# Optimization experiments

Measured on AMD Instinct MI355X. Metric: run time of the kernel, lower is better.

The kernel has to match this reference:

```python
import jax, jax.numpy as jnp
import numpy as np

TOP_K = 2
N_TOKENS = 8192
D_IN = 2048
HIDDEN = 2048
N_EXPERTS = 8


def setup_inputs() -> dict:
    key = jax.random.key(0)
    ks = jax.random.split(key, 3)
    # 0.001 stddev matches RandomNormal(mean=0, stddev=0.001) initializers
    x = jax.random.normal(ks[0], (N_TOKENS, D_IN), dtype=jnp.float32)
    Wg = jax.random.normal(ks[1], (D_IN, N_EXPERTS), dtype=jnp.float32) * 0.001
    bg = jnp.zeros((N_EXPERTS,), dtype=jnp.float32)
    We = jax.random.normal(ks[2], (N_EXPERTS, D_IN, HIDDEN), dtype=jnp.float32) * 0.001
    be = jnp.zeros((N_EXPERTS, HIDDEN), dtype=jnp.float32)
    return {"x": x, "Wg": Wg, "bg": bg, "We": We, "be": be}


def reference(x, Wg, bg, We, be):
    # Gating: dense -> softmax over experts
    gating = jax.nn.softmax(x @ Wg + bg, axis=-1)          # [N, E]
    top_w, top_i = jax.lax.top_k(gating, TOP_K)            # [N, K] each
    # Dense all-expert compute (as in the original: every expert runs on every token)
    expert_out = jnp.einsum('nd,edh->neh', x, We) + be      # [N, E, H]
    # Gather the top-k expert outputs per token and combine with gating weights
    sel = jnp.take_along_axis(expert_out, top_i[:, :, None], axis=1)  # [N, K, H]
    combined = jnp.sum(sel * top_w[:, :, None], axis=1)    # [N, H]
    return combined
```

## Files before the change

kernel.cpp:

```cpp
#include <hip/hip_runtime.h>
#include <hip/hip_bf16.h>

#define N_TOKENS 8192
#define D_IN     2048
#define HIDDEN   2048
#define N_EXP    8
#define CAP      N_TOKENS
#define GATE_BLOCKS 256
#define TPOSE_BLOCKS (N_EXP * 32 * 32)

typedef __bf16 bf16x8 __attribute__((ext_vector_type(8)));
typedef float  f32x4  __attribute__((ext_vector_type(4)));

#define OFF_CNT   0
#define OFF_TOK   4096
#define OFF_W     266240
#define OFF_XBF   1048576
#define OFF_WET   34603008

__device__ __forceinline__ unsigned short f2bf(float f) {
  unsigned int u = __builtin_bit_cast(unsigned int, f);
  u += 0x7fffu + ((u >> 16) & 1u);
  return (unsigned short)(u >> 16);
}

__device__ __forceinline__ void g2l16(const void* g, void* l) {
  __builtin_amdgcn_global_load_lds(
      (__attribute__((address_space(1))) void*)g,
      (__attribute__((address_space(3))) void*)l, 16, 0, 0);
}

union PrepSM {
  float tile[64][68];
  struct {
    int   lcnt[8];
    int   base[8];
    int   ltok[8][32];
    float lw[8][32];
  } g;
};

__global__ __launch_bounds__(256) void prep_kernel(
    const float* __restrict__ x, const float* __restrict__ Wg,
    const float* __restrict__ bg, const float* __restrict__ We,
    unsigned short* __restrict__ xbf, unsigned short* __restrict__ wet,
    int* __restrict__ cnt, int* __restrict__ btok, float* __restrict__ bw)
{
  __shared__ PrepSM sm;
  const int tid = threadIdx.x;

  if (blockIdx.x >= GATE_BLOCKS) {
    const int id = blockIdx.x - GATE_BLOCKS;
    const int e  = id >> 10;
    const int rem = id & 1023;
    const int d0 = (rem >> 5) << 6;
    const int h0 = (rem & 31) << 6;
    const int r  = tid >> 2;
    const int g  = tid & 3;

    const float* src = We + ((size_t)e * D_IN + d0 + r) * HIDDEN + h0 + g * 16;
#pragma unroll
    for (int i = 0; i < 4; ++i)
      *(float4*)&sm.tile[r][g * 16 + i * 4] = *(const float4*)(src + i * 4);
    __syncthreads();

    union { unsigned short s[16]; uint4 q[2]; } u;
#pragma unroll
    for (int i = 0; i < 16; ++i) u.s[i] = f2bf(sm.tile[g * 16 + i][r]);
    uint4* dst = (uint4*)(wet + ((size_t)e * HIDDEN + h0 + r) * D_IN + d0 + g * 16);
    dst[0] = u.q[0];
    dst[1] = u.q[1];
    return;
  }

  const int lane = tid & 63;
  const int wid  = tid >> 6;
  if (tid < 8) sm.g.lcnt[tid] = 0;
  __syncthreads();

  const int tb = blockIdx.x * 32 + wid * 8;
  for (int tk = 0; tk < 8; ++tk) {
    const int n = tb + tk;
    const float* xr = x + (size_t)n * D_IN;
    unsigned short* xbr = xbf + (size_t)n * D_IN;

#pragma unroll
    for (int c = 0; c < 8; ++c) {
      const int d = c * 256 + lane * 4;
      float4 xv = *(const float4*)(xr + d);
      uint2 pk;
      pk.x = (unsigned int)f2bf(xv.x) | ((unsigned int)f2bf(xv.y) << 16);
      pk.y = (unsigned int)f2bf(xv.z) | ((unsigned int)f2bf(xv.w) << 16);
      *(uint2*)(xbr + d) = pk;
    }

    float acc[8];
#pragma unroll
    for (int e = 0; e < 8; ++e) acc[e] = 0.f;
#pragma unroll 4
    for (int c = 0; c < 32; ++c) {
      const int d = c * 64 + lane;
      const float xv = xr[d];
      const float4 g0 = *(const float4*)(Wg + (size_t)d * 8);
      const float4 g1 = *(const float4*)(Wg + (size_t)d * 8 + 4);
      acc[0] += xv * g0.x; acc[1] += xv * g0.y;
      acc[2] += xv * g0.z; acc[3] += xv * g0.w;
      acc[4] += xv * g1.x; acc[5] += xv * g1.y;
      acc[6] += xv * g1.z; acc[7] += xv * g1.w;
    }
#pragma unroll
    for (int e = 0; e < 8; ++e) {
      float v = acc[e];
      v += __shfl_down(v, 32); v += __shfl_down(v, 16); v += __shfl_down(v, 8);
      v += __shfl_down(v, 4);  v += __shfl_down(v, 2);  v += __shfl_down(v, 1);
      acc[e] = v;
    }

    if (lane == 0) {
      float lg[8], p[8];
      float mx = -1e30f;
#pragma unroll
      for (int e = 0; e < 8; ++e) { lg[e] = acc[e] + bg[e]; mx = fmaxf(mx, lg[e]); }
      float s = 0.f;
#pragma unroll
      for (int e = 0; e < 8; ++e) { p[e] = expf(lg[e] - mx); s += p[e]; }
      const float inv = 1.f / s;
      int e1 = 0;
#pragma unroll
      for (int e = 1; e < 8; ++e) if (lg[e] > lg[e1]) e1 = e;
      int e2 = (e1 == 0) ? 1 : 0;
#pragma unroll
      for (int e = 0; e < 8; ++e) if (e != e1 && lg[e] > lg[e2]) e2 = e;

      const int s1 = atomicAdd(&sm.g.lcnt[e1], 1);
      sm.g.ltok[e1][s1] = n;  sm.g.lw[e1][s1] = p[e1] * inv;
      const int s2 = atomicAdd(&sm.g.lcnt[e2], 1);
      sm.g.ltok[e2][s2] = n;  sm.g.lw[e2][s2] = p[e2] * inv;
    }
  }
  __syncthreads();

  if (tid < 8) sm.g.base[tid] = atomicAdd(&cnt[tid * 32], sm.g.lcnt[tid]);
  __syncthreads();

  const int e = tid >> 5, i = tid & 31;
  if (i < sm.g.lcnt[e]) {
    const int o = e * CAP + sm.g.base[e] + i;
    btok[o] = sm.g.ltok[e][i];
    bw[o]   = sm.g.lw[e][i];
  }
}

__global__ __launch_bounds__(256, 4) void moe_gemm(
    const unsigned short* __restrict__ xbf, const unsigned short* __restrict__ wet,
    const float* __restrict__ be, const int* __restrict__ cnt,
    const int* __restrict__ btok, const float* __restrict__ bw,
    float* __restrict__ out)
{
  const int e  = blockIdx.z;
  const int M  = cnt[e * 32];
  const int m0 = blockIdx.y * 128;
  if (m0 >= M) return;
  const int h0 = blockIdx.x * 128;

  __shared__ __align__(16) unsigned short As[128 * 64];
  __shared__ __align__(16) unsigned short Bs[128 * 64];

  const int tid  = threadIdx.x;
  const int wid  = tid >> 6;
  const int lane = tid & 63;
  const int wm   = wid >> 1;
  const int wn   = wid & 1;

  const int* etok = btok + e * CAP;
  const float* ew = bw + e * CAP;

  const int kcs = (((lane & 7) ^ (lane >> 3)) * 8);

  size_t asrc[4], bsrc[4];
#pragma unroll
  for (int j = 0; j < 4; ++j) {
    const int c = wid * 4 + j;
    const int r = c * 8 + (lane >> 3);
    int ar = m0 + r;
    if (ar >= M) ar = m0;
    const int tok = etok[ar];
    asrc[j] = (size_t)tok * D_IN + kcs;
    bsrc[j] = ((size_t)e * HIDDEN + h0 + r) * D_IN + kcs;
  }

  f32x4 acc[4][4];
#pragma unroll
  for (int i = 0; i < 4; ++i)
#pragma unroll
    for (int j = 0; j < 4; ++j) acc[i][j] = (f32x4){0.f, 0.f, 0.f, 0.f};

  for (int k0 = 0; k0 < D_IN; k0 += 64) {
    __syncthreads();
#pragma unroll
    for (int j = 0; j < 4; ++j)
      g2l16(xbf + asrc[j] + k0, &As[(wid * 4 + j) * 512]);
#pragma unroll
    for (int j = 0; j < 4; ++j)
      g2l16(wet + bsrc[j] + k0, &Bs[(wid * 4 + j) * 512]);
    __syncthreads();

#pragma unroll
    for (int kh = 0; kh < 2; ++kh) {
      bf16x8 af[4], bfr[4];
#pragma unroll
      for (int fm = 0; fm < 4; ++fm) {
        const int row = wm * 64 + fm * 16 + (lane & 15);
        const int kc  = kh * 4 + (lane >> 4);
        af[fm] = __builtin_bit_cast(bf16x8,
            *(const uint4*)(As + row * 64 + ((kc ^ (row & 7)) * 8)));
      }
#pragma unroll
      for (int fn = 0; fn < 4; ++fn) {
        const int row = wn * 64 + fn * 16 + (lane & 15);
        const int kc  = kh * 4 + (lane >> 4);
        bfr[fn] = __builtin_bit_cast(bf16x8,
            *(const uint4*)(Bs + row * 64 + ((kc ^ (row & 7)) * 8)));
      }
#pragma unroll
      for (int fm = 0; fm < 4; ++fm)
#pragma unroll
        for (int fn = 0; fn < 4; ++fn)
          acc[fm][fn] = __builtin_amdgcn_mfma_f32_16x16x32_bf16(
              af[fm], bfr[fn], acc[fm][fn], 0, 0, 0);
    }
  }

  float bias[4];
#pragma unroll
  for (int fn = 0; fn < 4; ++fn)
    bias[fn] = be[e * HIDDEN + h0 + wn * 64 + fn * 16 + (lane & 15)];

#pragma unroll
  for (int fm = 0; fm < 4; ++fm) {
    const int rbase = m0 + wm * 64 + fm * 16 + (lane >> 4) * 4;
#pragma unroll
    for (int reg = 0; reg < 4; ++reg) {
      const int r = rbase + reg;
      if (r < M) {
        const int tok = etok[r];
        const float w = ew[r];
        float* orow = out + (size_t)tok * HIDDEN + h0 + wn * 64 + (lane & 15);
#pragma unroll
        for (int fn = 0; fn < 4; ++fn)
          atomicAdd(orow + fn * 16, w * (acc[fm][fn][reg] + bias[fn]));
      }
    }
  }
}

extern "C" void kernel_launch(void* const* d_in, const int* in_sizes, int n_in,
                              void* d_out, int out_size, void* d_ws, size_t ws_size,
                              hipStream_t stream) {
  const float* x  = (const float*)d_in[0];
  const float* Wg = (const float*)d_in[1];
  const float* bg = (const float*)d_in[2];
  const float* We = (const float*)d_in[3];
  const float* be = (const float*)d_in[4];
  float* out = (float*)d_out;

  char* ws = (char*)d_ws;
  int*            cnt  = (int*)(ws + OFF_CNT);
  int*            btok = (int*)(ws + OFF_TOK);
  float*          bw   = (float*)(ws + OFF_W);
  unsigned short* xbf  = (unsigned short*)(ws + OFF_XBF);
  unsigned short* wet  = (unsigned short*)(ws + OFF_WET);

  hipMemsetAsync(d_out, 0, (size_t)out_size * sizeof(float), stream);
  hipMemsetAsync(cnt, 0, 8 * 32 * sizeof(int), stream);

  prep_kernel<<<GATE_BLOCKS + TPOSE_BLOCKS, 256, 0, stream>>>(
      x, Wg, bg, We, xbf, wet, cnt, btok, bw);
  moe_gemm<<<dim3(HIDDEN / 128, N_TOKENS / 128, N_EXP), 256, 0, stream>>>(
      xbf, wet, be, cnt, btok, bw, out);
}
```

Before: 530.9 us.

## Double-buffer LDS tiles in MoE GEMM with prefetch two steps ahead

Converts the GEMM main loop to a double-buffered LDS pipeline. Direct global-to-LDS loads for tile t+2 are issued right after the fragments of tile t are read into registers, so the MFMAs run while the next tiles are in flight. It uses explicit vmcnt/lgkmcnt waits, raw barriers, sched_barriers and setprio around the MFMA block. LDS use doubles and launch bounds drop from 4 to 2 blocks per CU, which can reduce occupancy. The last two iterations issue wasted loads that wrap back to k=0.

```diff
diff --git a/kernel.cpp b/kernel.cpp
--- a/kernel.cpp
+++ b/kernel.cpp
@@ -151,7 +151,7 @@
   }
 }
 
-__global__ __launch_bounds__(256, 4) void moe_gemm(
+__global__ __launch_bounds__(256, 2) void moe_gemm(
     const unsigned short* __restrict__ xbf, const unsigned short* __restrict__ wet,
     const float* __restrict__ be, const int* __restrict__ cnt,
     const int* __restrict__ btok, const float* __restrict__ bw,
@@ -163,8 +163,8 @@
   if (m0 >= M) return;
   const int h0 = blockIdx.x * 128;
 
-  __shared__ __align__(16) unsigned short As[128 * 64];
-  __shared__ __align__(16) unsigned short Bs[128 * 64];
+  __shared__ __align__(16) unsigned short As[2][128 * 64];
+  __shared__ __align__(16) unsigned short Bs[2][128 * 64];
 
   const int tid  = threadIdx.x;
   const int wid  = tid >> 6;
@@ -195,40 +195,74 @@
 #pragma unroll
     for (int j = 0; j < 4; ++j) acc[i][j] = (f32x4){0.f, 0.f, 0.f, 0.f};
 
-  for (int k0 = 0; k0 < D_IN; k0 += 64) {
-    __syncthreads();
-#pragma unroll
-    for (int j = 0; j < 4; ++j)
-      g2l16(xbf + asrc[j] + k0, &As[(wid * 4 + j) * 512]);
-#pragma unroll
-    for (int j = 0; j < 4; ++j)
-      g2l16(wet + bsrc[j] + k0, &Bs[(wid * 4 + j) * 512]);
-    __syncthreads();
-
+#pragma unroll
+  for (int j = 0; j < 4; ++j)
+    g2l16(xbf + asrc[j], &As[0][(wid * 4 + j) * 512]);
+#pragma unroll
+  for (int j = 0; j < 4; ++j)
+    g2l16(wet + bsrc[j], &Bs[0][(wid * 4 + j) * 512]);
+  asm volatile("" ::: "memory");
+#pragma unroll
+  for (int j = 0; j < 4; ++j)
+    g2l16(xbf + asrc[j] + 64, &As[1][(wid * 4 + j) * 512]);
+#pragma unroll
+  for (int j = 0; j < 4; ++j)
+    g2l16(wet + bsrc[j] + 64, &Bs[1][(wid * 4 + j) * 512]);
+
+#pragma unroll 1
+  for (int t = 0; t < D_IN / 64; ++t) {
+    const int cur = t & 1;
+    const unsigned short* Ab = &As[cur][0];
+    const unsigned short* Bb = &Bs[cur][0];
+
+    asm volatile("s_waitcnt vmcnt(8)" ::: "memory");
+    __builtin_amdgcn_s_barrier();
+    __builtin_amdgcn_sched_barrier(0);
+
+    bf16x8 af[4][2], bfr[4][2];
 #pragma unroll
     for (int kh = 0; kh < 2; ++kh) {
-      bf16x8 af[4], bfr[4];
 #pragma unroll
       for (int fm = 0; fm < 4; ++fm) {
         const int row = wm * 64 + fm * 16 + (lane & 15);
         const int kc  = kh * 4 + (lane >> 4);
-        af[fm] = __builtin_bit_cast(bf16x8,
-            *(const uint4*)(As + row * 64 + ((kc ^ (row & 7)) * 8)));
+        af[fm][kh] = __builtin_bit_cast(bf16x8,
+            *(const uint4*)(Ab + row * 64 + ((kc ^ (row & 7)) * 8)));
       }
 #pragma unroll
       for (int fn = 0; fn < 4; ++fn) {
         const int row = wn * 64 + fn * 16 + (lane & 15);
         const int kc  = kh * 4 + (lane >> 4);
-        bfr[fn] = __builtin_bit_cast(bf16x8,
-            *(const uint4*)(Bs + row * 64 + ((kc ^ (row & 7)) * 8)));
+        bfr[fn][kh] = __builtin_bit_cast(bf16x8,
+            *(const uint4*)(Bb + row * 64 + ((kc ^ (row & 7)) * 8)));
       }
+    }
+
+    asm volatile("s_waitcnt lgkmcnt(0)" ::: "memory");
+    __builtin_amdgcn_sched_barrier(0);
+    __builtin_amdgcn_s_barrier();
+    __builtin_amdgcn_sched_barrier(0);
+
+    int kp = (t + 2) * 64;
+    if (kp >= D_IN) kp = 0;
+#pragma unroll
+    for (int j = 0; j < 4; ++j)
+      g2l16(xbf + asrc[j] + kp, &As[cur][(wid * 4 + j) * 512]);
+#pragma unroll
+    for (int j = 0; j < 4; ++j)
+      g2l16(wet + bsrc[j] + kp, &Bs[cur][(wid * 4 + j) * 512]);
+    __builtin_amdgcn_sched_barrier(0);
+
+    __builtin_amdgcn_s_setprio(1);
+#pragma unroll
+    for (int kh = 0; kh < 2; ++kh)
 #pragma unroll
       for (int fm = 0; fm < 4; ++fm)
 #pragma unroll
         for (int fn = 0; fn < 4; ++fn)
           acc[fm][fn] = __builtin_amdgcn_mfma_f32_16x16x32_bf16(
-              af[fm], bfr[fn], acc[fm][fn], 0, 0, 0);
-    }
+              af[fm][kh], bfr[fn][kh], acc[fm][fn], 0, 0, 0);
+    __builtin_amdgcn_s_setprio(0);
   }
 
   float bias[4];
```

Measured after the change: 576.6 us. +8.6%, slower.

## Enlarge MoE GEMM tiles to 256x256 with multi-stage LDS prefetch pipeline

Applied to the files above, without the earlier changes.

Rewrites the grouped expert GEMM to use 512-thread blocks computing 256x256 output tiles with 8 waves. The K loop now runs over 32-wide k-slices held in a four-slot LDS ring (double buffer by two slices), issuing async global-to-LDS loads several slices ahead and interleaving them with MFMA bursts under explicit waitcnt and barrier control. The aim is to hide global load latency and raise arithmetic intensity per LDS byte. Costs include higher register pressure from 32 accumulator tiles, coarser tiles that waste work on partial expert groups, and a fragile hand-scheduled pipeline.

```diff
diff --git a/kernel.cpp b/kernel.cpp
--- a/kernel.cpp
+++ b/kernel.cpp
@@ -151,7 +151,7 @@
   }
 }
 
-__global__ __launch_bounds__(256, 4) void moe_gemm(
+__global__ __launch_bounds__(512, 2) void moe_gemm(
     const unsigned short* __restrict__ xbf, const unsigned short* __restrict__ wet,
     const float* __restrict__ be, const int* __restrict__ cnt,
     const int* __restrict__ btok, const float* __restrict__ bw,
@@ -159,76 +159,107 @@
 {
   const int e  = blockIdx.z;
   const int M  = cnt[e * 32];
-  const int m0 = blockIdx.y * 128;
+  const int m0 = blockIdx.y * 256;
   if (m0 >= M) return;
-  const int h0 = blockIdx.x * 128;
-
-  __shared__ __align__(16) unsigned short As[128 * 64];
-  __shared__ __align__(16) unsigned short Bs[128 * 64];
+  const int h0 = blockIdx.x * 256;
+
+  __shared__ __align__(16) unsigned short As[2][2][256 * 32];
+  __shared__ __align__(16) unsigned short Bs[2][2][256 * 32];
 
   const int tid  = threadIdx.x;
   const int wid  = tid >> 6;
   const int lane = tid & 63;
-  const int wm   = wid >> 1;
-  const int wn   = wid & 1;
+  const int wm   = wid >> 2;
+  const int wn   = wid & 3;
 
   const int* etok = btok + e * CAP;
   const float* ew = bw + e * CAP;
 
-  const int kcs = (((lane & 7) ^ (lane >> 3)) * 8);
-
-  size_t asrc[4], bsrc[4];
-#pragma unroll
-  for (int j = 0; j < 4; ++j) {
-    const int c = wid * 4 + j;
-    const int r = c * 8 + (lane >> 3);
+  const int kqs = (((lane & 3) ^ ((lane >> 3) & 3)) * 8);
+
+  size_t asrc[2], bsrc[2];
+#pragma unroll
+  for (int j = 0; j < 2; ++j) {
+    const int r = (wid * 2 + j) * 16 + (lane >> 2);
     int ar = m0 + r;
     if (ar >= M) ar = m0;
-    const int tok = etok[ar];
-    asrc[j] = (size_t)tok * D_IN + kcs;
-    bsrc[j] = ((size_t)e * HIDDEN + h0 + r) * D_IN + kcs;
-  }
-
-  f32x4 acc[4][4];
-#pragma unroll
-  for (int i = 0; i < 4; ++i)
+    asrc[j] = (size_t)etok[ar] * D_IN + kqs;
+    bsrc[j] = ((size_t)e * HIDDEN + h0 + r) * D_IN + kqs;
+  }
+
+  f32x4 acc[8][4];
+#pragma unroll
+  for (int i = 0; i < 8; ++i)
 #pragma unroll
     for (int j = 0; j < 4; ++j) acc[i][j] = (f32x4){0.f, 0.f, 0.f, 0.f};
 
-  for (int k0 = 0; k0 < D_IN; k0 += 64) {
-    __syncthreads();
-#pragma unroll
-    for (int j = 0; j < 4; ++j)
-      g2l16(xbf + asrc[j] + k0, &As[(wid * 4 + j) * 512]);
-#pragma unroll
-    for (int j = 0; j < 4; ++j)
-      g2l16(wet + bsrc[j] + k0, &Bs[(wid * 4 + j) * 512]);
-    __syncthreads();
-
-#pragma unroll
-    for (int kh = 0; kh < 2; ++kh) {
-      bf16x8 af[4], bfr[4];
-#pragma unroll
-      for (int fm = 0; fm < 4; ++fm) {
-        const int row = wm * 64 + fm * 16 + (lane & 15);
-        const int kc  = kh * 4 + (lane >> 4);
-        af[fm] = __builtin_bit_cast(bf16x8,
-            *(const uint4*)(As + row * 64 + ((kc ^ (row & 7)) * 8)));
-      }
-#pragma unroll
-      for (int fn = 0; fn < 4; ++fn) {
-        const int row = wn * 64 + fn * 16 + (lane & 15);
-        const int kc  = kh * 4 + (lane >> 4);
-        bfr[fn] = __builtin_bit_cast(bf16x8,
-            *(const uint4*)(Bs + row * 64 + ((kc ^ (row & 7)) * 8)));
-      }
-#pragma unroll
-      for (int fm = 0; fm < 4; ++fm)
-#pragma unroll
-        for (int fn = 0; fn < 4; ++fn)
-          acc[fm][fn] = __builtin_amdgcn_mfma_f32_16x16x32_bf16(
-              af[fm], bfr[fn], acc[fm][fn], 0, 0, 0);
-    }
+  bf16x8 af[8], bfr[4];
+
+#define SG_A(db_, ks_, ko_) {                                                  \
+    const int ko = ((ko_) < D_IN) ? (ko_) : 0;                                 \
+    g2l16(xbf + asrc[0] + ko, &As[db_][ks_][(wid * 2 + 0) * 512]);             \
+    g2l16(xbf + asrc[1] + ko, &As[db_][ks_][(wid * 2 + 1) * 512]);             \
+    asm volatile("" ::: "memory"); }
+#define SG_B(db_, ks_, ko_) {                                                  \
+    const int ko = ((ko_) < D_IN) ? (ko_) : 0;                                 \
+    g2l16(wet + bsrc[0] + ko, &Bs[db_][ks_][(wid * 2 + 0) * 512]);             \
+    g2l16(wet + bsrc[1] + ko, &Bs[db_][ks_][(wid * 2 + 1) * 512]);             \
+    asm volatile("" ::: "memory"); }
+#define RD_A(db_, ks_) {                                                       \
+    _Pragma("unroll")                                                          \
+    for (int fm = 0; fm < 8; ++fm) {                                           \
+      const int row = wm * 128 + fm * 16 + (lane & 15);                        \
+      af[fm] = __builtin_bit_cast(bf16x8, *(const uint4*)(                     \
+          &As[db_][ks_][row * 32 + (((lane >> 4) ^ ((row >> 1) & 3)) * 8)]));} }
+#define RD_B(db_, ks_, nh_) {                                                  \
+    _Pragma("unroll")                                                          \
+    for (int q = 0; q < 2; ++q) {                                              \
+      const int fn = (nh_) * 2 + q;                                            \
+      const int row = wn * 64 + fn * 16 + (lane & 15);                         \
+      bfr[fn] = __builtin_bit_cast(bf16x8, *(const uint4*)(                    \
+          &Bs[db_][ks_][row * 32 + (((lane >> 4) ^ ((row >> 1) & 3)) * 8)]));} }
+#define VM8()  asm volatile("s_waitcnt vmcnt(8)" ::: "memory")
+#define SBAR() { __builtin_amdgcn_sched_barrier(0);                            \
+                 __builtin_amdgcn_s_barrier();                                 \
+                 __builtin_amdgcn_sched_barrier(0); }
+#define LGKM0() { asm volatile("s_waitcnt lgkmcnt(0)" ::: "memory");           \
+                  __builtin_amdgcn_sched_barrier(0); }
+#define MM(nh_) {                                                              \
+    __builtin_amdgcn_s_setprio(1);                                             \
+    _Pragma("unroll")                                                          \
+    for (int fm = 0; fm < 8; ++fm) {                                           \
+      acc[fm][(nh_) * 2] = __builtin_amdgcn_mfma_f32_16x16x32_bf16(            \
+          af[fm], bfr[(nh_) * 2], acc[fm][(nh_) * 2], 0, 0, 0);                \
+      acc[fm][(nh_) * 2 + 1] = __builtin_amdgcn_mfma_f32_16x16x32_bf16(        \
+          af[fm], bfr[(nh_) * 2 + 1], acc[fm][(nh_) * 2 + 1], 0, 0, 0); }      \
+    __builtin_amdgcn_s_setprio(0); }
+
+  SG_A(0, 0, 0);  SG_B(0, 0, 0);
+  SG_A(0, 1, 32); SG_B(0, 1, 32);
+  SG_A(1, 0, 64); SG_B(1, 0, 64);
+  VM8();
+  SBAR();
+
+#pragma unroll 1
+  for (int it = 0; it < 16; ++it) {
+    const int kb = it * 128;
+
+    RD_A(0, 0); RD_B(0, 0, 0); SG_A(1, 1, kb + 96);
+    SBAR(); LGKM0(); MM(0);
+    RD_B(0, 0, 1); SG_B(1, 1, kb + 96); VM8();
+    SBAR(); LGKM0(); MM(1);
+    RD_A(0, 1); RD_B(0, 1, 0); SG_A(0, 0, kb + 128);
+    SBAR(); LGKM0(); MM(0);
+    RD_B(0, 1, 1); SG_B(0, 0, kb + 128); VM8();
+    SBAR(); LGKM0(); MM(1);
+    RD_A(1, 0); RD_B(1, 0, 0); SG_A(0, 1, kb + 160);
+    SBAR(); LGKM0(); MM(0);
+    RD_B(1, 0, 1); SG_B(0, 1, kb + 160); VM8();
+    SBAR(); LGKM0(); MM(1);
+    RD_A(1, 1); RD_B(1, 1, 0); SG_A(1, 0, kb + 192);
+    SBAR(); LGKM0(); MM(0);
+    RD_B(1, 1, 1); SG_B(1, 0, kb + 192); VM8();
+    SBAR(); LGKM0(); MM(1);
   }
 
   float bias[4];
@@ -237,8 +268,8 @@
     bias[fn] = be[e * HIDDEN + h0 + wn * 64 + fn * 16 + (lane & 15)];
 
 #pragma unroll
-  for (int fm = 0; fm < 4; ++fm) {
-    const int rbase = m0 + wm * 64 + fm * 16 + (lane >> 4) * 4;
+  for (int fm = 0; fm < 8; ++fm) {
+    const int rbase = m0 + wm * 128 + fm * 16 + (lane >> 4) * 4;
 #pragma unroll
     for (int reg = 0; reg < 4; ++reg) {
       const int r = rbase + reg;
@@ -252,6 +283,14 @@
       }
     }
   }
+#undef SG_A
+#undef SG_B
+#undef RD_A
+#undef RD_B
+#undef VM8
+#undef SBAR
+#undef LGKM0
+#undef MM
 }
 
 extern "C" void kernel_launch(void* const* d_in, const int* in_sizes, int n_in,
@@ -276,6 +315,6 @@
 
   prep_kernel<<<GATE_BLOCKS + TPOSE_BLOCKS, 256, 0, stream>>>(
       x, Wg, bg, We, xbf, wet, cnt, btok, bw);
-  moe_gemm<<<dim3(HIDDEN / 128, N_TOKENS / 128, N_EXP), 256, 0, stream>>>(
+  moe_gemm<<<dim3(HIDDEN / 256, N_TOKENS / 256, N_EXP), 512, 0, stream>>>(
       xbf, wet, be, cnt, btok, bw, out);
 }
```

Result: slower. 569.4 us (+7.3%).

## Replace output atomics with slot-separated plain stores plus combine pass; swizzle grid

Applied to the files above, without the earlier changes.

Each token's second-choice expert is tagged in the token index, so the GEMM epilogue writes its result with plain stores into a separate workspace buffer. First-choice results go straight into the output. A combine kernel then adds the two buffers, which removes the output memset and the float atomicAdds. The block index is also remapped to interleave experts across consecutive blocks. The cost is an extra 64MB buffer plus a full read-modify-write pass, and the new path only runs when the workspace is large enough.

```diff
diff --git a/kernel.cpp b/kernel.cpp
--- a/kernel.cpp
+++ b/kernel.cpp
@@ -17,6 +17,8 @@
 #define OFF_W     266240
 #define OFF_XBF   1048576
 #define OFF_WET   34603008
+#define OFF_P1    101711872ull
+#define WS_NEED   (OFF_P1 + (size_t)N_TOKENS * HIDDEN * 4)
 
 __device__ __forceinline__ unsigned short f2bf(float f) {
   unsigned int u = __builtin_bit_cast(unsigned int, f);
@@ -133,9 +135,9 @@
       for (int e = 0; e < 8; ++e) if (e != e1 && lg[e] > lg[e2]) e2 = e;
 
       const int s1 = atomicAdd(&sm.g.lcnt[e1], 1);
-      sm.g.ltok[e1][s1] = n;  sm.g.lw[e1][s1] = p[e1] * inv;
+      sm.g.ltok[e1][s1] = n;              sm.g.lw[e1][s1] = p[e1] * inv;
       const int s2 = atomicAdd(&sm.g.lcnt[e2], 1);
-      sm.g.ltok[e2][s2] = n;  sm.g.lw[e2][s2] = p[e2] * inv;
+      sm.g.ltok[e2][s2] = n | (1 << 13);  sm.g.lw[e2][s2] = p[e2] * inv;
     }
   }
   __syncthreads();
@@ -151,17 +153,21 @@
   }
 }
 
+template <int SLOTTED>
 __global__ __launch_bounds__(256, 4) void moe_gemm(
     const unsigned short* __restrict__ xbf, const unsigned short* __restrict__ wet,
     const float* __restrict__ be, const int* __restrict__ cnt,
     const int* __restrict__ btok, const float* __restrict__ bw,
-    float* __restrict__ out)
+    float* __restrict__ out, float* __restrict__ p1)
 {
-  const int e  = blockIdx.z;
-  const int M  = cnt[e * 32];
-  const int m0 = blockIdx.y * 128;
+  const int flat = blockIdx.x + (blockIdx.y << 4) + (blockIdx.z << 10);
+  const int swz  = ((flat & 7) << 10) + (flat >> 3);
+  const int e    = swz >> 10;
+  const int h0   = ((swz >> 6) & 15) << 7;
+  const int m0   = (swz & 63) << 7;
+
+  const int M = cnt[e * 32];
   if (m0 >= M) return;
-  const int h0 = blockIdx.x * 128;
 
   __shared__ __align__(16) unsigned short As[128 * 64];
   __shared__ __align__(16) unsigned short Bs[128 * 64];
@@ -184,7 +190,7 @@
     const int r = c * 8 + (lane >> 3);
     int ar = m0 + r;
     if (ar >= M) ar = m0;
-    const int tok = etok[ar];
+    const int tok = etok[ar] & 8191;
     asrc[j] = (size_t)tok * D_IN + kcs;
     bsrc[j] = ((size_t)e * HIDDEN + h0 + r) * D_IN + kcs;
   }
@@ -243,14 +249,36 @@
     for (int reg = 0; reg < 4; ++reg) {
       const int r = rbase + reg;
       if (r < M) {
-        const int tok = etok[r];
+        const int tv  = etok[r];
+        const int tok = tv & 8191;
         const float w = ew[r];
-        float* orow = out + (size_t)tok * HIDDEN + h0 + wn * 64 + (lane & 15);
-#pragma unroll
-        for (int fn = 0; fn < 4; ++fn)
-          atomicAdd(orow + fn * 16, w * (acc[fm][fn][reg] + bias[fn]));
+        if (SLOTTED) {
+          float* dst = ((tv >> 13) ? p1 : out) +
+                       (size_t)tok * HIDDEN + h0 + wn * 64 + (lane & 15);
+#pragma unroll
+          for (int fn = 0; fn < 4; ++fn)
+            dst[fn * 16] = w * (acc[fm][fn][reg] + bias[fn]);
+        } else {
+          float* orow = out + (size_t)tok * HIDDEN + h0 + wn * 64 + (lane & 15);
+#pragma unroll
+          for (int fn = 0; fn < 4; ++fn)
+            atomicAdd(orow + fn * 16, w * (acc[fm][fn][reg] + bias[fn]));
+        }
       }
     }
+  }
+}
+
+__global__ __launch_bounds__(256) void combine_kernel(
+    float* __restrict__ out, const float* __restrict__ p1)
+{
+  const int stride = gridDim.x * 256;
+  for (int i = blockIdx.x * 256 + threadIdx.x;
+       i < N_TOKENS * HIDDEN / 4; i += stride) {
+    float4 a = ((const float4*)out)[i];
+    const float4 b = ((const float4*)p1)[i];
+    a.x += b.x; a.y += b.y; a.z += b.z; a.w += b.w;
+    ((float4*)out)[i] = a;
   }
 }
 
@@ -270,12 +298,23 @@
   float*          bw   = (float*)(ws + OFF_W);
   unsigned short* xbf  = (unsigned short*)(ws + OFF_XBF);
   unsigned short* wet  = (unsigned short*)(ws + OFF_WET);
-
-  hipMemsetAsync(d_out, 0, (size_t)out_size * sizeof(float), stream);
+  float*          p1   = (float*)(ws + OFF_P1);
+
+  const bool slotted = (ws_size >= WS_NEED);
+
   hipMemsetAsync(cnt, 0, 8 * 32 * sizeof(int), stream);
+  if (!slotted)
+    hipMemsetAsync(d_out, 0, (size_t)out_size * sizeof(float), stream);
 
   prep_kernel<<<GATE_BLOCKS + TPOSE_BLOCKS, 256, 0, stream>>>(
       x, Wg, bg, We, xbf, wet, cnt, btok, bw);
-  moe_gemm<<<dim3(HIDDEN / 128, N_TOKENS / 128, N_EXP), 256, 0, stream>>>(
-      xbf, wet, be, cnt, btok, bw, out);
-}
+
+  if (slotted) {
+    moe_gemm<1><<<dim3(HIDDEN / 128, N_TOKENS / 128, N_EXP), 256, 0, stream>>>(
+        xbf, wet, be, cnt, btok, bw, out, p1);
+    combine_kernel<<<2048, 256, 0, stream>>>(out, p1);
+  } else {
+    moe_gemm<0><<<dim3(HIDDEN / 128, N_TOKENS / 128, N_EXP), 256, 0, stream>>>(
+        xbf, wet, be, cnt, btok, bw, out, p1);
+  }
+}
```

After: 515.6 us. -2.9%, faster.
